# Performance work log

Measured on AMD Instinct MI355X. Metric: run time of the kernel, lower is better.

## Reference

```python
import jax, jax.numpy as jnp
import numpy as np

INC = 64; OUTC = 64; TS = 3; CS = 3; MAXN = 10; SIGMA = 2.0; STRIDE = 1
TAU = 0.1


def _gaussian_decay(length, max_val, sigma):
    x = np.arange(length, dtype=np.float32)
    y = max_val * np.exp(-x ** 2 / (2.0 * sigma ** 2))
    return (np.floor(y) + 1).astype(np.int64)


def _get_p_n(t_size, c_size, max_number, sigma):
    f_num = _gaussian_decay(t_size, max_number, sigma)
    c_num = _gaussian_decay(c_size, max_number, sigma)
    px, py = [], []
    for i in range(1, t_size):
        for _ in range(int(f_num[i])):
            px.append(0); py.append(i)
    for i in range(c_size):
        for _ in range(int(c_num[i])):
            px.append(i); py.append(0)
    f_number = int(f_num.sum()) - max_number - 1 if t_size > 0 else 0
    for i in range(c_size):
        for j in range(c_size):
            px.append(i); py.append(j)
    p_n = np.stack([np.array(px, np.float32), np.array(py, np.float32)], 0)  # (2, N)
    return p_n, f_number, p_n.shape[1] - f_number


def _conv(x, w, b, groups=1, pad=0):
    y = jax.lax.conv_general_dilated(
        x, w, (1, 1), [(pad, pad), (pad, pad)],
        dimension_numbers=('NCHW', 'OIHW', 'NCHW'), feature_group_count=groups)
    return y + b[None, :, None, None]


def _bilinear_sample_zeros(img, coords):
    # img (b,c,H,W); coords (b,N,h,w,2) pixel-space (x,y); zeros padding, align_corners=True
    b, c, H, W = img.shape
    x = coords[..., 0]; y = coords[..., 1]
    x0 = jnp.floor(x); y0 = jnp.floor(y)
    wx1 = x - x0; wy1 = y - y0

    def gather(yi, xi, wgt):
        valid = (xi >= 0) & (xi <= W - 1) & (yi >= 0) & (yi <= H - 1)
        xc = jnp.clip(xi, 0, W - 1).astype(jnp.int32)
        yc = jnp.clip(yi, 0, H - 1).astype(jnp.int32)
        vals = jax.vmap(lambda im, yy, xx: im[:, yy, xx])(img, yc, xc)  # (b,c,N,h,w)
        return vals * (wgt * valid.astype(img.dtype))[:, None]

    return (gather(y0, x0, (1 - wy1) * (1 - wx1)) + gather(y0, x0 + 1, (1 - wy1) * wx1)
            + gather(y0 + 1, x0, wy1 * (1 - wx1)) + gather(y0 + 1, x0 + 1, wy1 * wx1))


def setup_inputs() -> dict:
    key = jax.random.key(0)
    ks = jax.random.split(key, 12)
    p_n_np, f_num, c_num = _get_p_n(TS, CS, MAXN, SIGMA)
    N = p_n_np.shape[1]  # 52
    B, H, W = 4, 64, 64
    s = 0.05
    return {
        'x': jax.random.normal(ks[0], (B, INC, H, W), jnp.float32),
        'p_n': jnp.asarray(p_n_np),
        'dwf_w': jax.random.normal(ks[1], (INC, 1, 3, 3), jnp.float32) * s,
        'dwf_b': jnp.zeros((INC,), jnp.float32),
        'pwf_w': jax.random.normal(ks[2], (2 * f_num, INC, 1, 1), jnp.float32) * s,
        'pwf_b': jnp.zeros((2 * f_num,), jnp.float32),
        'dwc_w': jax.random.normal(ks[3], (INC, 1, 3, 3), jnp.float32) * s,
        'dwc_b': jnp.zeros((INC,), jnp.float32),
        'pwc_w': jax.random.normal(ks[4], (2 * c_num, INC, 1, 1), jnp.float32) * s,
        'pwc_b': jnp.zeros((2 * c_num,), jnp.float32),
        'dwm_w': jax.random.normal(ks[5], (INC, 1, 3, 3), jnp.float32) * s,
        'dwm_b': jnp.zeros((INC,), jnp.float32),
        'pwm_w': jax.random.normal(ks[6], (N + 1, INC, 1, 1), jnp.float32) * s,
        'pwm_b': jnp.zeros((N + 1,), jnp.float32),
        'pc_w': jax.random.normal(ks[7], (OUTC, INC, 1, 1), jnp.float32) * s,
        'pc_b': jnp.zeros((OUTC,), jnp.float32),
        'mlp_w1': jax.random.normal(ks[8], (OUTC, OUTC), jnp.float32) * s,
        'mlp_b1': jnp.zeros((OUTC,), jnp.float32),
        'mlp_w2': jax.random.normal(ks[9], (OUTC, OUTC), jnp.float32) * s,
        'mlp_b2': jnp.zeros((OUTC,), jnp.float32),
    }


def reference(x, p_n, dwf_w, dwf_b, pwf_w, pwf_b, dwc_w, dwc_b, pwc_w, pwc_b,
              dwm_w, dwm_b, pwm_w, pwm_b, pc_w, pc_b, mlp_w1, mlp_b1, mlp_w2, mlp_b2):
    b, c, H, W = x.shape
    N = p_n.shape[1]
    # learned per-pixel offsets (depthwise 3x3 + pointwise 1x1), concat f then c branch
    off_f = _conv(_conv(x, dwf_w, dwf_b, groups=c, pad=1), pwf_w, pwf_b)
    off_c = _conv(_conv(x, dwc_w, dwc_b, groups=c, pad=1), pwc_w, pwc_b)
    offset = jnp.concatenate([off_f, off_c], axis=1)  # (b, 2N, h, w)
    h, w = offset.shape[2], offset.shape[3]
    # modulation scores with learned sparsity threshold
    m = _conv(_conv(x, dwm_w, dwm_b, groups=c, pad=1), pwm_w, pwm_b)  # (b, N+1, h, w)
    sparsity = m[:, -1:]
    scores = m[:, :N]
    soft_mask = jax.nn.sigmoid((scores - sparsity) / TAU)
    mod = jax.nn.softmax(scores + jnp.log(soft_mask + 1e-10), axis=1)  # (b,N,h,w)
    # absolute sampling coordinates: base grid + fixed pattern p_n + learned offset
    dt = x.dtype
    gy, gx = jnp.meshgrid(jnp.arange(0, h * STRIDE, STRIDE, dtype=dt),
                          jnp.arange(0, w * STRIDE, STRIDE, dtype=dt), indexing='ij')
    grid = jnp.stack([gx, gy], -1)[None, None]            # (1,1,h,w,2)
    pn = p_n.T[None, :, None, None, :]                    # (1,N,1,1,2)
    off = offset.reshape(b, 2, N, h, w).transpose(0, 2, 3, 4, 1)  # (b,N,h,w,2)
    abs_c = grid + pn + off
    # normalize to [-1,1] then back to pixel space (grid_sample align_corners=True)
    nx = 2.0 * abs_c[..., 0] / (W - 1) - 1.0
    ny = 2.0 * abs_c[..., 1] / (H - 1) - 1.0
    coords = jnp.stack([(nx + 1.0) * 0.5 * (W - 1), (ny + 1.0) * 0.5 * (H - 1)], -1)
    sampled = _bilinear_sample_zeros(jax.lax.stop_gradient(x), coords)  # (b,c,N,h,w)
    agg = jnp.einsum('bcnhw,bnhw->bchw', sampled, mod)
    out = _conv(agg, pc_w, pc_b)  # 1x1 pointwise conv -> (b,outc,h,w)
    # per-pixel MLP over channels
    h1 = jax.nn.relu(jnp.einsum('bchw,dc->bdhw', out, mlp_w1) + mlp_b1[None, :, None, None])
    h2 = jnp.einsum('bchw,dc->bdhw', h1, mlp_w2) + mlp_b2[None, :, None, None]
    return h2 + x
```

## Files before the change

### kernel.cpp

```cpp
#include <hip/hip_runtime.h>
#include <hip/hip_fp16.h>
#include <cmath>

#define BB 4
#define HH 64
#define WW 64

#define OFFW  18560
#define SBW   25320
#define CMAP  28871
#define FLBC  30496
#define FLB   30497
#define POOLW 37154
#define TF_H  21760
#define TC_H  26880
#define TM_H  32000
#define AGG_H 69188
#define PCB_H 37120
#define H1_H  42240

typedef _Float16 f16x8 __attribute__((ext_vector_type(8)));
typedef float    f32x4 __attribute__((ext_vector_type(4)));

__global__ __launch_bounds__(256) void transpose_half(const float* __restrict__ x,
                                                      __half* __restrict__ xth) {
    int bid = blockIdx.x;
    int b = bid >> 6, y = bid & 63;
    __shared__ float tile[64][65];
    const float* xp = x + ((size_t)b * 64 * HH + y) * WW;
    #pragma unroll
    for (int k = 0; k < 16; ++k) {
        int idx = threadIdx.x + (k << 8);
        int c = idx >> 6, w = idx & 63;
        tile[c][w] = xp[(size_t)c * HH * WW + w];
    }
    __syncthreads();
    __half* op = xth + ((size_t)(b * HH + y) * WW) * 64;
    #pragma unroll
    for (int k = 0; k < 16; ++k) {
        int idx = threadIdx.x + (k << 8);
        int w = idx >> 6, c = idx & 63;
        op[(size_t)w * 64 + c] = __float2half(tile[c][w]);
    }
}

__device__ inline f32x4 tile_gemm64(const __half* PH, int actH,
                                    const float* __restrict__ W,
                                    const float* __restrict__ Bv,
                                    int m_t, int n_t, int lane) {
    const int row = m_t * 16 + (lane & 15);
    const int kg  = (lane >> 4) * 8;
    const float* wr = W + row * 64 + kg;
    float4 wa0 = *reinterpret_cast<const float4*>(wr);
    float4 wa1 = *reinterpret_cast<const float4*>(wr + 4);
    float4 wb0 = *reinterpret_cast<const float4*>(wr + 32);
    float4 wb1 = *reinterpret_cast<const float4*>(wr + 36);
    f16x8 a0, a1;
    a0[0]=(_Float16)wa0.x; a0[1]=(_Float16)wa0.y; a0[2]=(_Float16)wa0.z; a0[3]=(_Float16)wa0.w;
    a0[4]=(_Float16)wa1.x; a0[5]=(_Float16)wa1.y; a0[6]=(_Float16)wa1.z; a0[7]=(_Float16)wa1.w;
    a1[0]=(_Float16)wb0.x; a1[1]=(_Float16)wb0.y; a1[2]=(_Float16)wb0.z; a1[3]=(_Float16)wb0.w;
    a1[4]=(_Float16)wb1.x; a1[5]=(_Float16)wb1.y; a1[6]=(_Float16)wb1.z; a1[7]=(_Float16)wb1.w;
    const int px = n_t * 16 + (lane & 15);
    f16x8 b0 = *reinterpret_cast<const f16x8*>(&PH[actH + px * 80 + kg]);
    f16x8 b1 = *reinterpret_cast<const f16x8*>(&PH[actH + px * 80 + 32 + kg]);
    f32x4 d;
    const int r0 = m_t * 16 + ((lane >> 4) << 2);
    #pragma unroll
    for (int r = 0; r < 4; ++r) d[r] = Bv[r0 + r];
    d = __builtin_amdgcn_mfma_f32_16x16x32_f16(a0, b0, d, 0, 0, 0);
    d = __builtin_amdgcn_mfma_f32_16x16x32_f16(a1, b1, d, 0, 0, 0);
    return d;
}

__global__ __launch_bounds__(1024, 4) void crossd_main(
    const __half* __restrict__ xth, const float* __restrict__ x,
    const float* __restrict__ p_n,
    const float* __restrict__ dwf_w, const float* __restrict__ dwf_b,
    const float* __restrict__ pwf_w, const float* __restrict__ pwf_b,
    const float* __restrict__ dwc_w, const float* __restrict__ dwc_b,
    const float* __restrict__ pwc_w, const float* __restrict__ pwc_b,
    const float* __restrict__ dwm_w, const float* __restrict__ dwm_b,
    const float* __restrict__ pwm_w, const float* __restrict__ pwm_b,
    const float* __restrict__ pc_w, const float* __restrict__ pc_b,
    const float* __restrict__ w1, const float* __restrict__ b1,
    const float* __restrict__ w2, const float* __restrict__ b2,
    float* __restrict__ out)
{
    __shared__ float P[POOLW];
    uint32_t* PU = reinterpret_cast<uint32_t*>(P);
    __half*   PH = reinterpret_cast<__half*>(P);
    const int tid  = threadIdx.x;
    const int lane = tid & 63;
    const int wv   = __builtin_amdgcn_readfirstlane(tid >> 6);
    const int b = blockIdx.x >> 6, y = blockIdx.x & 63;
    const int ry0 = min(max(y - 1, 0), 59);
    const __half* xbh = xth + (size_t)b * (HH * WW * 64);
    const uint2* xb2 = reinterpret_cast<const uint2*>(xbh);

    {
        for (int idx = tid; idx < 5 * 64 * 16; idx += 1024) {
            int j = idx >> 10;
            int rem = idx & 1023;
            int px = rem >> 4, c4v = idx & 15;
            *reinterpret_cast<uint2*>(&PH[(j * 64 + px) * 68 + c4v * 4]) =
                xb2[(((ry0 + j) << 6) + px) * 16 + c4v];
        }
        for (int i = tid; i < 25 * 65 + 1; i += 1024) P[CMAP + i] = 0.0f;
    }
    __syncthreads();

    {
        const int c = lane;
        float wf9[9], wc9[9], wm9[9];
        #pragma unroll
        for (int k9 = 0; k9 < 9; ++k9) {
            wf9[k9] = dwf_w[c * 9 + k9];
            wc9[k9] = dwc_w[c * 9 + k9];
            wm9[k9] = dwm_w[c * 9 + k9];
        }
        const float bf = dwf_b[c], bc = dwc_b[c], bm = dwm_b[c];
        #pragma unroll
        for (int i = 0; i < 4; ++i) {
            const int px = wv * 4 + i;
            float af = bf, ac = bc, am = bm;
            #pragma unroll
            for (int dy = 0; dy < 3; ++dy) {
                int yy = y + dy - 1;
                if (yy < 0 || yy >= HH) continue;
                int j = yy - ry0;
                #pragma unroll
                for (int dx = 0; dx < 3; ++dx) {
                    int xx = px + dx - 1;
                    if (xx < 0 || xx >= WW) continue;
                    float v = __half2float(PH[(j * 64 + xx) * 68 + c]);
                    int k = dy * 3 + dx;
                    af = fmaf(v, wf9[k], af);
                    ac = fmaf(v, wc9[k], ac);
                    am = fmaf(v, wm9[k], am);
                }
            }
            PH[TF_H + px * 80 + c] = __float2half(af);
            PH[TC_H + px * 80 + c] = __float2half(ac);
            PH[TM_H + px * 80 + c] = __float2half(am);
        }
    }
    __syncthreads();

    {
        const int n_t = wv & 3;
        const int g   = wv >> 2;
        #pragma unroll
        for (int t = 0; t < 3; ++t) {
            const int m_t = g + t * 4;
            if (m_t < 11) {
                const float *Wb, *Bvb; int rows, actH, r0b, br;
                if (m_t < 2)      { Wb=pwf_w; Bvb=pwf_b; rows=32; actH=TF_H; r0b=m_t*16;     br=0; }
                else if (m_t < 7) { Wb=pwc_w; Bvb=pwc_b; rows=72; actH=TC_H; r0b=(m_t-2)*16; br=1; }
                else              { Wb=pwm_w; Bvb=pwm_b; rows=53; actH=TM_H; r0b=(m_t-7)*16; br=2; }
                const int rl  = min(r0b + (lane & 15), rows - 1);
                const int kg  = (lane >> 4) * 8;
                const float* wr = Wb + rl * 64 + kg;
                float4 wa0 = *reinterpret_cast<const float4*>(wr);
                float4 wa1 = *reinterpret_cast<const float4*>(wr + 4);
                float4 wb0 = *reinterpret_cast<const float4*>(wr + 32);
                float4 wb1 = *reinterpret_cast<const float4*>(wr + 36);
                f16x8 a0, a1;
                a0[0]=(_Float16)wa0.x; a0[1]=(_Float16)wa0.y; a0[2]=(_Float16)wa0.z; a0[3]=(_Float16)wa0.w;
                a0[4]=(_Float16)wa1.x; a0[5]=(_Float16)wa1.y; a0[6]=(_Float16)wa1.z; a0[7]=(_Float16)wa1.w;
                a1[0]=(_Float16)wb0.x; a1[1]=(_Float16)wb0.y; a1[2]=(_Float16)wb0.z; a1[3]=(_Float16)wb0.w;
                a1[4]=(_Float16)wb1.x; a1[5]=(_Float16)wb1.y; a1[6]=(_Float16)wb1.z; a1[7]=(_Float16)wb1.w;
                const int px = n_t * 16 + (lane & 15);
                f16x8 b0 = *reinterpret_cast<const f16x8*>(&PH[actH + px * 80 + kg]);
                f16x8 b1 = *reinterpret_cast<const f16x8*>(&PH[actH + px * 80 + 32 + kg]);
                f32x4 d;
                const int rr0 = r0b + ((lane >> 4) << 2);
                #pragma unroll
                for (int r = 0; r < 4; ++r) d[r] = Bvb[min(rr0 + r, rows - 1)];
                d = __builtin_amdgcn_mfma_f32_16x16x32_f16(a0, b0, d, 0, 0, 0);
                d = __builtin_amdgcn_mfma_f32_16x16x32_f16(a1, b1, d, 0, 0, 0);
                #pragma unroll
                for (int r = 0; r < 4; ++r) {
                    const int rb = rr0 + r;
                    if (rb < rows) {
                        const float v = d[r];
                        if (br == 2)      P[SBW + rb * 67 + px] = v;
                        else {
                            int og = (br == 0) ? rb : 32 + rb;
                            P[OFFW + og * 65 + px] = v;
                        }
                    }
                }
            }
        }
    }
    __syncthreads();

    #pragma unroll
    for (int i = 0; i < 4; ++i) {
        const int px = wv * 4 + i;
        const float sp = P[SBW + 52 * 67 + px];
        float z = -1e30f;
        if (lane < 52) {
            float s  = P[SBW + lane * 67 + px];
            float sg = 1.0f / (1.0f + __expf(-(s - sp) * 10.0f));
            z = s + __logf(sg + 1e-10f);
        }
        float mx = z;
        #pragma unroll
        for (int d = 32; d >= 1; d >>= 1) mx = fmaxf(mx, __shfl_xor(mx, d));
        float e = (lane < 52) ? __expf(z - mx) : 0.0f;
        float sm = e;
        #pragma unroll
        for (int d = 32; d >= 1; d >>= 1) sm += __shfl_xor(sm, d);
        if (lane < 52) P[SBW + lane * 67 + px] = e / sm;
    }
    __syncthreads();

    {
        const int ppx = tid & 63;
        const int g   = tid >> 6;
        for (int n = g; n < 52; n += 16) {
            float sx = (float)ppx + p_n[n]      + P[OFFW + n * 65 + ppx];
            float sy = (float)y   + p_n[52 + n] + P[OFFW + (52 + n) * 65 + ppx];
            float mo = P[SBW + n * 67 + ppx];
            float x0f = floorf(sx), y0f = floorf(sy);
            float wx1 = sx - x0f, wy1 = sy - y0f;
            float wx0 = 1.0f - wx1, wy0 = 1.0f - wy1;
            int xi = (int)x0f, yi = (int)y0f;
            bool vx0 = (xi >= 0)  & (xi <= 63);
            bool vx1 = (xi >= -1) & (xi <= 62);
            bool vy0 = (yi >= 0)  & (yi <= 63);
            bool vy1 = (yi >= -1) & (yi <= 62);
            float m00 = (vy0 & vx0) ? mo * wy0 * wx0 : 0.0f;
            float m01 = (vy0 & vx1) ? mo * wy0 * wx1 : 0.0f;
            float m10 = (vy1 & vx0) ? mo * wy1 * wx0 : 0.0f;
            float m11 = (vy1 & vx1) ? mo * wy1 * wx1 : 0.0f;
            const int i0 = xi - ppx + 1, j0 = yi - ry0;
            #define PUSH(m, jj, ii, gx, gy) \
                if (m != 0.0f) { \
                    if ((jj) >= 0 && (jj) <= 4 && (ii) >= 0 && (ii) <= 4) { \
                        atomicAdd(&P[CMAP + ((jj) * 5 + (ii)) * 65 + ppx], m); \
                    } else { \
                        uint32_t a = (uint32_t)((gy) * 64 + (gx)); \
                        uint32_t sl = atomicAdd(&PU[FLBC], 1u); \
                        if (sl < 2048u) { \
                            PU[FLB + sl * 2]     = a | ((uint32_t)ppx << 16); \
                            PU[FLB + sl * 2 + 1] = __float_as_uint(m); \
                        } \
                    } \
                }
            PUSH(m00, j0,     i0,     xi,     yi);
            PUSH(m01, j0,     i0 + 1, xi + 1, yi);
            PUSH(m10, j0 + 1, i0,     xi,     yi + 1);
            PUSH(m11, j0 + 1, i0 + 1, xi + 1, yi + 1);
            #undef PUSH
        }
    }
    __syncthreads();

    {
        const int sub = lane >> 4;
        const int c4  = lane & 15;
        const int spx = wv * 4 + sub;
        int co[5];
        #pragma unroll
        for (int i = 0; i < 5; ++i) co[i] = min(max(spx - 1 + i, 0), 63);
        float4 agg = make_float4(0.f, 0.f, 0.f, 0.f);
        #pragma unroll
        for (int j = 0; j < 5; ++j) {
            #pragma unroll
            for (int i = 0; i < 5; ++i) {
                float w = P[CMAP + (j * 5 + i) * 65 + spx];
                uint2 u = *reinterpret_cast<const uint2*>(&PH[(j * 64 + co[i]) * 68 + c4 * 4]);
                __half2 hlo = *reinterpret_cast<const __half2*>(&u.x);
                __half2 hhi = *reinterpret_cast<const __half2*>(&u.y);
                float2 flo = __half22float2(hlo), fhi = __half22float2(hhi);
                agg.x = fmaf(w, flo.x, agg.x); agg.y = fmaf(w, flo.y, agg.y);
                agg.z = fmaf(w, fhi.x, agg.z); agg.w = fmaf(w, fhi.y, agg.w);
            }
        }
        const int cnt = min((int)PU[FLBC], 2048);
        for (int e = 0; e < cnt; ++e) {
            uint32_t ea = PU[FLB + e * 2];
            float m = __uint_as_float(PU[FLB + e * 2 + 1]);
            if ((int)(ea >> 16) == spx) {
                uint2 u = xb2[(ea & 0xFFFFu) * 16 + c4];
                __half2 hlo = *reinterpret_cast<const __half2*>(&u.x);
                __half2 hhi = *reinterpret_cast<const __half2*>(&u.y);
                float2 flo = __half22float2(hlo), fhi = __half22float2(hhi);
                agg.x = fmaf(m, flo.x, agg.x); agg.y = fmaf(m, flo.y, agg.y);
                agg.z = fmaf(m, fhi.x, agg.z); agg.w = fmaf(m, fhi.y, agg.w);
            }
        }
        __half2 p0 = __floats2half2_rn(agg.x, agg.y);
        __half2 p1 = __floats2half2_rn(agg.z, agg.w);
        uint2 pk2;
        pk2.x = *reinterpret_cast<uint32_t*>(&p0);
        pk2.y = *reinterpret_cast<uint32_t*>(&p1);
        *reinterpret_cast<uint2*>(&PH[AGG_H + spx * 80 + c4 * 4]) = pk2;
    }
    __syncthreads();

    {
        f32x4 d = tile_gemm64(PH, AGG_H, pc_w, pc_b, wv >> 2, wv & 3, lane);
        const int px = (wv & 3) * 16 + (lane & 15);
        const int o0 = (wv >> 2) * 16 + ((lane >> 4) << 2);
        __half2 p0 = __floats2half2_rn(d[0], d[1]);
        __half2 p1 = __floats2half2_rn(d[2], d[3]);
        uint2 pk2;
        pk2.x = *reinterpret_cast<uint32_t*>(&p0);
        pk2.y = *reinterpret_cast<uint32_t*>(&p1);
        *reinterpret_cast<uint2*>(&PH[PCB_H + px * 80 + o0]) = pk2;
    }
    __syncthreads();

    {
        f32x4 d = tile_gemm64(PH, PCB_H, w1, b1, wv >> 2, wv & 3, lane);
        #pragma unroll
        for (int r = 0; r < 4; ++r) d[r] = fmaxf(d[r], 0.0f);
        const int px = (wv & 3) * 16 + (lane & 15);
        const int o0 = (wv >> 2) * 16 + ((lane >> 4) << 2);
        __half2 p0 = __floats2half2_rn(d[0], d[1]);
        __half2 p1 = __floats2half2_rn(d[2], d[3]);
        uint2 pk2;
        pk2.x = *reinterpret_cast<uint32_t*>(&p0);
        pk2.y = *reinterpret_cast<uint32_t*>(&p1);
        *reinterpret_cast<uint2*>(&PH[H1_H + px * 80 + o0]) = pk2;
    }
    __syncthreads();

    {
        f32x4 d = tile_gemm64(PH, H1_H, w2, b2, wv >> 2, wv & 3, lane);
        const int px = (wv & 3) * 16 + (lane & 15);
        const int o0 = (wv >> 2) * 16 + ((lane >> 4) << 2);
        #pragma unroll
        for (int r = 0; r < 4; ++r) {
            const int o = o0 + r;
            size_t idx = (((size_t)b * 64 + o) * 64 + y) * 64 + px;
            out[idx] = d[r] + x[idx];
        }
    }
}

extern "C" void kernel_launch(void* const* d_in, const int* in_sizes, int n_in,
                              void* d_out, int out_size, void* d_ws, size_t ws_size,
                              hipStream_t stream) {
    const float* x     = (const float*)d_in[0];
    const float* p_n   = (const float*)d_in[1];
    const float* dwf_w = (const float*)d_in[2];
    const float* dwf_b = (const float*)d_in[3];
    const float* pwf_w = (const float*)d_in[4];
    const float* pwf_b = (const float*)d_in[5];
    const float* dwc_w = (const float*)d_in[6];
    const float* dwc_b = (const float*)d_in[7];
    const float* pwc_w = (const float*)d_in[8];
    const float* pwc_b = (const float*)d_in[9];
    const float* dwm_w = (const float*)d_in[10];
    const float* dwm_b = (const float*)d_in[11];
    const float* pwm_w = (const float*)d_in[12];
    const float* pwm_b = (const float*)d_in[13];
    const float* pc_w  = (const float*)d_in[14];
    const float* pc_b  = (const float*)d_in[15];
    const float* w1    = (const float*)d_in[16];
    const float* b1    = (const float*)d_in[17];
    const float* w2    = (const float*)d_in[18];
    const float* b2    = (const float*)d_in[19];

    __half* xth = (__half*)d_ws;
    float* outp = (float*)d_out;

    hipLaunchKernelGGL(transpose_half, dim3(BB * HH), dim3(256), 0, stream, x, xth);
    hipLaunchKernelGGL(crossd_main, dim3(BB * HH), dim3(1024), 0, stream,
                       xth, x, p_n,
                       dwf_w, dwf_b, pwf_w, pwf_b,
                       dwc_w, dwc_b, pwc_w, pwc_b,
                       dwm_w, dwm_b, pwm_w, pwm_b,
                       pc_w, pc_b, w1, b1, w2, b2, outp);
}
```

Baseline: 50.41 us.

## Split each image row into two half-row blocks of 512 threads

```diff
diff --git a/kernel.cpp b/kernel.cpp
--- a/kernel.cpp
+++ b/kernel.cpp
@@ -6,18 +6,19 @@
 #define HH 64
 #define WW 64
 
-#define OFFW  18560
-#define SBW   25320
-#define CMAP  28871
-#define FLBC  30496
-#define FLB   30497
-#define POOLW 37154
-#define TF_H  21760
-#define TC_H  26880
-#define TM_H  32000
-#define AGG_H 69188
-#define PCB_H 37120
-#define H1_H  42240
+#define OFFW  9960
+#define SBW   13392
+#define CMAP  15247
+#define FLBC  16072
+#define FLB   16073
+#define POOLW 18377
+#define WIN_H 0
+#define TF_H  12240
+#define TC_H  14800
+#define TM_H  17360
+#define AGG_H 34194
+#define PCB_H 19920
+#define H1_H  22480
 
 typedef _Float16 f16x8 __attribute__((ext_vector_type(8)));
 typedef float    f32x4 __attribute__((ext_vector_type(4)));
@@ -72,7 +73,7 @@
     return d;
 }
 
-__global__ __launch_bounds__(1024, 4) void crossd_main(
+__global__ __launch_bounds__(512, 4) void crossd_main(
     const __half* __restrict__ xth, const float* __restrict__ x,
     const float* __restrict__ p_n,
     const float* __restrict__ dwf_w, const float* __restrict__ dwf_b,
@@ -92,20 +93,23 @@
     const int tid  = threadIdx.x;
     const int lane = tid & 63;
     const int wv   = __builtin_amdgcn_readfirstlane(tid >> 6);
-    const int b = blockIdx.x >> 6, y = blockIdx.x & 63;
+    const int bid = blockIdx.x;
+    const int xh = bid & 1, y = (bid >> 1) & 63, b = bid >> 7;
+    const int x0 = xh << 5;
     const int ry0 = min(max(y - 1, 0), 59);
     const __half* xbh = xth + (size_t)b * (HH * WW * 64);
     const uint2* xb2 = reinterpret_cast<const uint2*>(xbh);
 
     {
-        for (int idx = tid; idx < 5 * 64 * 16; idx += 1024) {
-            int j = idx >> 10;
-            int rem = idx & 1023;
-            int px = rem >> 4, c4v = idx & 15;
-            *reinterpret_cast<uint2*>(&PH[(j * 64 + px) * 68 + c4v * 4]) =
-                xb2[(((ry0 + j) << 6) + px) * 16 + c4v];
-        }
-        for (int i = tid; i < 25 * 65 + 1; i += 1024) P[CMAP + i] = 0.0f;
+        for (int idx = tid; idx < 5 * 36 * 16; idx += 512) {
+            int j = idx / 576;
+            int rem = idx - j * 576;
+            int col = rem >> 4, c4v = idx & 15;
+            int gcol = min(max(x0 - 1 + col, 0), 63);
+            *reinterpret_cast<uint2*>(&PH[(j * 36 + col) * 68 + c4v * 4]) =
+                xb2[(((ry0 + j) << 6) + gcol) * 16 + c4v];
+        }
+        for (int i = tid; i < 25 * 33 + 1; i += 512) P[CMAP + i] = 0.0f;
     }
     __syncthreads();
 
@@ -121,7 +125,8 @@
         const float bf = dwf_b[c], bc = dwc_b[c], bm = dwm_b[c];
         #pragma unroll
         for (int i = 0; i < 4; ++i) {
-            const int px = wv * 4 + i;
+            const int pl = wv * 4 + i;
+            const int pg = x0 + pl;
             float af = bf, ac = bc, am = bm;
             #pragma unroll
             for (int dy = 0; dy < 3; ++dy) {
@@ -130,25 +135,26 @@
                 int j = yy - ry0;
                 #pragma unroll
                 for (int dx = 0; dx < 3; ++dx) {
-                    int xx = px + dx - 1;
+                    int xx = pg + dx - 1;
                     if (xx < 0 || xx >= WW) continue;
-                    float v = __half2float(PH[(j * 64 + xx) * 68 + c]);
+                    int co = xx - x0 + 1;
+                    float v = __half2float(PH[(j * 36 + co) * 68 + c]);
                     int k = dy * 3 + dx;
                     af = fmaf(v, wf9[k], af);
                     ac = fmaf(v, wc9[k], ac);
                     am = fmaf(v, wm9[k], am);
                 }
             }
-            PH[TF_H + px * 80 + c] = __float2half(af);
-            PH[TC_H + px * 80 + c] = __float2half(ac);
-            PH[TM_H + px * 80 + c] = __float2half(am);
-        }
-    }
-    __syncthreads();
-
-    {
-        const int n_t = wv & 3;
-        const int g   = wv >> 2;
+            PH[TF_H + pl * 80 + c] = __float2half(af);
+            PH[TC_H + pl * 80 + c] = __float2half(ac);
+            PH[TM_H + pl * 80 + c] = __float2half(am);
+        }
+    }
+    __syncthreads();
+
+    {
+        const int n_t = wv & 1;
+        const int g   = wv >> 1;
         #pragma unroll
         for (int t = 0; t < 3; ++t) {
             const int m_t = g + t * 4;
@@ -183,10 +189,10 @@
                     const int rb = rr0 + r;
                     if (rb < rows) {
                         const float v = d[r];
-                        if (br == 2)      P[SBW + rb * 67 + px] = v;
+                        if (br == 2)      P[SBW + rb * 35 + px] = v;
                         else {
                             int og = (br == 0) ? rb : 32 + rb;
-                            P[OFFW + og * 65 + px] = v;
+                            P[OFFW + og * 33 + px] = v;
                         }
                     }
                 }
@@ -195,13 +201,13 @@
     }
     __syncthreads();
 
-    #pragma unroll
+    #pragma unroll 1
     for (int i = 0; i < 4; ++i) {
-        const int px = wv * 4 + i;
-        const float sp = P[SBW + 52 * 67 + px];
+        const int pl = wv * 4 + i;
+        const float sp = P[SBW + 52 * 35 + pl];
         float z = -1e30f;
         if (lane < 52) {
-            float s  = P[SBW + lane * 67 + px];
+            float s  = P[SBW + lane * 35 + pl];
             float sg = 1.0f / (1.0f + __expf(-(s - sp) * 10.0f));
             z = s + __logf(sg + 1e-10f);
         }
@@ -212,17 +218,11 @@
         float sm = e;
         #pragma unroll
         for (int d = 32; d >= 1; d >>= 1) sm += __shfl_xor(sm, d);
-        if (lane < 52) P[SBW + lane * 67 + px] = e / sm;
-    }
-    __syncthreads();
-
-    {
-        const int ppx = tid & 63;
-        const int g   = tid >> 6;
-        for (int n = g; n < 52; n += 16) {
-            float sx = (float)ppx + p_n[n]      + P[OFFW + n * 65 + ppx];
-            float sy = (float)y   + p_n[52 + n] + P[OFFW + (52 + n) * 65 + ppx];
-            float mo = P[SBW + n * 67 + ppx];
+        if (lane < 52) {
+            const float mo = e / sm;
+            const int pg = x0 + pl;
+            float sx = (float)pg + p_n[lane]      + P[OFFW + lane * 33 + pl];
+            float sy = (float)y  + p_n[52 + lane] + P[OFFW + (52 + lane) * 33 + pl];
             float x0f = floorf(sx), y0f = floorf(sy);
             float wx1 = sx - x0f, wy1 = sy - y0f;
             float wx0 = 1.0f - wx1, wy0 = 1.0f - wy1;
@@ -235,16 +235,16 @@
             float m01 = (vy0 & vx1) ? mo * wy0 * wx1 : 0.0f;
             float m10 = (vy1 & vx0) ? mo * wy1 * wx0 : 0.0f;
             float m11 = (vy1 & vx1) ? mo * wy1 * wx1 : 0.0f;
-            const int i0 = xi - ppx + 1, j0 = yi - ry0;
+            const int i0 = xi - pg + 1, j0 = yi - ry0;
             #define PUSH(m, jj, ii, gx, gy) \
                 if (m != 0.0f) { \
                     if ((jj) >= 0 && (jj) <= 4 && (ii) >= 0 && (ii) <= 4) { \
-                        atomicAdd(&P[CMAP + ((jj) * 5 + (ii)) * 65 + ppx], m); \
+                        atomicAdd(&P[CMAP + ((jj) * 5 + (ii)) * 33 + pl], m); \
                     } else { \
                         uint32_t a = (uint32_t)((gy) * 64 + (gx)); \
                         uint32_t sl = atomicAdd(&PU[FLBC], 1u); \
-                        if (sl < 2048u) { \
-                            PU[FLB + sl * 2]     = a | ((uint32_t)ppx << 16); \
+                        if (sl < 512u) { \
+                            PU[FLB + sl * 2]     = a | ((uint32_t)pl << 16); \
                             PU[FLB + sl * 2 + 1] = __float_as_uint(m); \
                         } \
                     } \
@@ -262,16 +262,17 @@
         const int sub = lane >> 4;
         const int c4  = lane & 15;
         const int spx = wv * 4 + sub;
+        const int spg = x0 + spx;
         int co[5];
         #pragma unroll
-        for (int i = 0; i < 5; ++i) co[i] = min(max(spx - 1 + i, 0), 63);
+        for (int i = 0; i < 5; ++i) co[i] = min(max(spg - 1 + i, 0), 63) - x0 + 1;
         float4 agg = make_float4(0.f, 0.f, 0.f, 0.f);
         #pragma unroll
         for (int j = 0; j < 5; ++j) {
             #pragma unroll
             for (int i = 0; i < 5; ++i) {
-                float w = P[CMAP + (j * 5 + i) * 65 + spx];
-                uint2 u = *reinterpret_cast<const uint2*>(&PH[(j * 64 + co[i]) * 68 + c4 * 4]);
+                float w = P[CMAP + (j * 5 + i) * 33 + spx];
+                uint2 u = *reinterpret_cast<const uint2*>(&PH[(j * 36 + co[i]) * 68 + c4 * 4]);
                 __half2 hlo = *reinterpret_cast<const __half2*>(&u.x);
                 __half2 hhi = *reinterpret_cast<const __half2*>(&u.y);
                 float2 flo = __half22float2(hlo), fhi = __half22float2(hhi);
@@ -279,7 +280,7 @@
                 agg.z = fmaf(w, fhi.x, agg.z); agg.w = fmaf(w, fhi.y, agg.w);
             }
         }
-        const int cnt = min((int)PU[FLBC], 2048);
+        const int cnt = min((int)PU[FLBC], 512);
         for (int e = 0; e < cnt; ++e) {
             uint32_t ea = PU[FLB + e * 2];
             float m = __uint_as_float(PU[FLB + e * 2 + 1]);
@@ -302,9 +303,9 @@
     __syncthreads();
 
     {
-        f32x4 d = tile_gemm64(PH, AGG_H, pc_w, pc_b, wv >> 2, wv & 3, lane);
-        const int px = (wv & 3) * 16 + (lane & 15);
-        const int o0 = (wv >> 2) * 16 + ((lane >> 4) << 2);
+        f32x4 d = tile_gemm64(PH, AGG_H, pc_w, pc_b, wv >> 1, wv & 1, lane);
+        const int px = (wv & 1) * 16 + (lane & 15);
+        const int o0 = (wv >> 1) * 16 + ((lane >> 4) << 2);
         __half2 p0 = __floats2half2_rn(d[0], d[1]);
         __half2 p1 = __floats2half2_rn(d[2], d[3]);
         uint2 pk2;
@@ -315,11 +316,11 @@
     __syncthreads();
 
     {
-        f32x4 d = tile_gemm64(PH, PCB_H, w1, b1, wv >> 2, wv & 3, lane);
+        f32x4 d = tile_gemm64(PH, PCB_H, w1, b1, wv >> 1, wv & 1, lane);
         #pragma unroll
         for (int r = 0; r < 4; ++r) d[r] = fmaxf(d[r], 0.0f);
-        const int px = (wv & 3) * 16 + (lane & 15);
-        const int o0 = (wv >> 2) * 16 + ((lane >> 4) << 2);
+        const int px = (wv & 1) * 16 + (lane & 15);
+        const int o0 = (wv >> 1) * 16 + ((lane >> 4) << 2);
         __half2 p0 = __floats2half2_rn(d[0], d[1]);
         __half2 p1 = __floats2half2_rn(d[2], d[3]);
         uint2 pk2;
@@ -330,13 +331,13 @@
     __syncthreads();
 
     {
-        f32x4 d = tile_gemm64(PH, H1_H, w2, b2, wv >> 2, wv & 3, lane);
-        const int px = (wv & 3) * 16 + (lane & 15);
-        const int o0 = (wv >> 2) * 16 + ((lane >> 4) << 2);
+        f32x4 d = tile_gemm64(PH, H1_H, w2, b2, wv >> 1, wv & 1, lane);
+        const int px = (wv & 1) * 16 + (lane & 15);
+        const int o0 = (wv >> 1) * 16 + ((lane >> 4) << 2);
         #pragma unroll
         for (int r = 0; r < 4; ++r) {
             const int o = o0 + r;
-            size_t idx = (((size_t)b * 64 + o) * 64 + y) * 64 + px;
+            size_t idx = (((size_t)b * 64 + o) * 64 + y) * 64 + x0 + px;
             out[idx] = d[r] + x[idx];
         }
     }
@@ -370,7 +371,7 @@
     float* outp = (float*)d_out;
 
     hipLaunchKernelGGL(transpose_half, dim3(BB * HH), dim3(256), 0, stream, x, xth);
-    hipLaunchKernelGGL(crossd_main, dim3(BB * HH), dim3(1024), 0, stream,
+    hipLaunchKernelGGL(crossd_main, dim3(BB * HH * 2), dim3(512), 0, stream,
                        xth, x, p_n,
                        dwf_w, dwf_b, pwf_w, pwf_b,
                        dwc_w, dwc_b, pwc_w, pwc_b,
```

Measured after the change: 48.83 us. 3.1% less time.
